# Kernel optimization log

Measured on AMD Instinct MI355X. Metric: run time of the kernel, lower is better.

Reference implementation:

```python
import jax, jax.numpy as jnp
import numpy as np
from jax import lax

NPOINT = 1024
RADIUS = 0.2
NSAMPLE = 32


def fps(xyz, npoint):
    """Furthest point sampling on one cloud. xyz: (N,3) -> (npoint,) int32."""
    n = xyz.shape[0]
    init_d = jnp.full((n,), 1e10, xyz.dtype)

    def body(carry, _):
        dists, last_idx = carry
        last = xyz[last_idx]
        d = jnp.sum((xyz - last) ** 2, axis=-1)
        dists = jnp.minimum(dists, d)
        nxt = jnp.argmax(dists).astype(jnp.int32)
        return (dists, nxt), nxt

    (_, _), idxs = lax.scan(body, (init_d, jnp.int32(0)), None, length=npoint - 1)
    return jnp.concatenate([jnp.zeros((1,), jnp.int32), idxs])


def ball_query(xyz, new_xyz, radius, nsample):
    """First `nsample` points of xyz within `radius` of each center (pad with first hit).
    xyz: (N,3), new_xyz: (S,3) -> (S,nsample) int32."""
    n = xyz.shape[0]
    d2 = jnp.sum((new_xyz[:, None, :] - xyz[None, :, :]) ** 2, axis=-1)  # (S,N)
    cand = jnp.where(d2 < radius * radius, jnp.arange(n, dtype=jnp.int32)[None, :], n)
    idx = jnp.sort(cand, axis=1)[:, :nsample]                            # (S,K)
    first = jnp.where(idx[:, :1] == n, 0, idx[:, :1])
    return jnp.where(idx == n, first, idx)


def setup_inputs() -> dict:
    key = jax.random.key(0)
    ks = jax.random.split(key, 8)
    C_in = 64 + 3  # features + relative xyz
    W1 = jax.random.normal(ks[0], (64, C_in), jnp.float32) * (1.0 / np.sqrt(C_in))
    b1 = jnp.zeros((64,), jnp.float32)
    W2 = jax.random.normal(ks[1], (128, 64), jnp.float32) * (1.0 / np.sqrt(64))
    b2 = jnp.zeros((128,), jnp.float32)
    W3 = jax.random.normal(ks[2], (256, 128), jnp.float32) * (1.0 / np.sqrt(128))
    b3 = jnp.zeros((256,), jnp.float32)
    xyz = jax.random.uniform(ks[3], (8, 4096, 3), jnp.float32)
    features = jax.random.normal(ks[4], (8, 4096, 64), jnp.float32)
    return {"xyz": xyz, "features": features, "W1": W1, "b1": b1,
            "W2": W2, "b2": b2, "W3": W3, "b3": b3}


def reference(xyz, features, W1, b1, W2, b2, W3, b3):
    def per_batch(xyz_b, feat_b):
        fps_idx = fps(xyz_b, NPOINT)                      # (S,)
        new_xyz = xyz_b[fps_idx]                          # (S,3)
        idx = ball_query(xyz_b, new_xyz, RADIUS, NSAMPLE)  # (S,K)
        g_xyz = xyz_b[idx] - new_xyz[:, None, :]          # (S,K,3) relative coords
        g_feat = feat_b[idx]                              # (S,K,C)
        g = jnp.concatenate([g_xyz, g_feat], axis=-1)     # (S,K,3+C)
        x = jnp.transpose(g, (2, 0, 1))                   # (C',S,K)
        for W, b in ((W1, b1), (W2, b2), (W3, b3)):       # 1x1 conv + ReLU stack
            x = jax.nn.relu(jnp.einsum('oc,csk->osk', W, x) + b[:, None, None])
        return new_xyz, jnp.max(x, axis=-1), fps_idx      # max-pool over nsample

    new_xyz, new_features, sample_inds = jax.vmap(per_batch)(xyz, features)
    return new_xyz, new_features, sample_inds
```

## Files before the change

kernel.cpp:

```cpp
#include <hip/hip_runtime.h>
#include <stdint.h>

#define N_PTS 4096
#define S_PTS 1024
#define K_SAMP 32

typedef __attribute__((ext_vector_type(8))) short bf16x8;
typedef __attribute__((ext_vector_type(4))) float f32x4;
typedef __attribute__((ext_vector_type(2))) float f32x2;

#define GT1_S 104
#define GT2_S 72
#define GT3_S 136

__device__ __forceinline__ short f2b(float f){
  unsigned u = __float_as_uint(f);
  u = u + 0x7fffu + ((u >> 16) & 1u);
  return (short)(u >> 16);
}

#define DPP_QUAD_XOR1 0xB1
#define DPP_QUAD_XOR2 0x4E
#define DPP_ROW_HMIRR 0x141
#define DPP_ROW_MIRR  0x140
#define DPP_ROW_BC15  0x142
#define DPP_ROW_BC31  0x143

template<int CTRL>
__device__ __forceinline__ float fstep(float v){
  int o = __builtin_amdgcn_update_dpp(__float_as_int(v), __float_as_int(v),
                                      CTRL, 0xF, 0xF, false);
  return fmaxf(v, __int_as_float(o));
}
template<int CTRL>
__device__ __forceinline__ unsigned ustep(unsigned v){
  unsigned o = (unsigned)__builtin_amdgcn_update_dpp((int)v, (int)v,
                                                     CTRL, 0xF, 0xF, false);
  return o < v ? o : v;
}
__device__ __forceinline__ unsigned long long umax64(unsigned long long a,
                                                     unsigned long long b){
  return a > b ? a : b;
}

__global__ __launch_bounds__(256) void fps_kernel(const float* __restrict__ xyz,
                                                  float* __restrict__ out_newxyz,
                                                  float* __restrict__ out_inds){
#pragma clang fp contract(off)
  __shared__ float4 c4[N_PTS];
  __shared__ float4 logxyz[S_PTS];
  __shared__ __align__(16) unsigned long long slots[2][4];
  const int b = blockIdx.x;
  const int t = threadIdx.x;
  const int lane = t & 63;
  const int w = t >> 6;
  const float* xb = xyz + (size_t)b * N_PTS * 3;

  f32x2 px2[8], py2[8], pz2[8], dist2[8];
#pragma unroll
  for (int j = 0; j < 16; ++j){
    int p = j * 256 + t;
    float x = xb[p*3+0], y = xb[p*3+1], z = xb[p*3+2];
    px2[j>>1][j&1] = x; py2[j>>1][j&1] = y; pz2[j>>1][j&1] = z;
    dist2[j>>1][j&1] = 1e10f;
    c4[p] = make_float4(x, y, z, 0.0f);
  }
  __syncthreads();

  float lx, ly, lz;
  { float4 c0 = c4[0]; lx = c0.x; ly = c0.y; lz = c0.z; }
  if (t == 0) logxyz[0] = make_float4(lx, ly, lz, 0.0f);

  for (int it = 1; it < S_PTS; ++it){
    f32x2 vlx = {lx, lx}, vly = {ly, ly}, vlz = {lz, lz};
    f32x2 bq2[8];
#pragma unroll
    for (int q = 0; q < 8; ++q){
      f32x2 dx = px2[q] - vlx;
      f32x2 dy = py2[q] - vly;
      f32x2 dz = pz2[q] - vlz;
      f32x2 m1 = dx * dx;
      f32x2 m2 = dy * dy;
      f32x2 m3 = dz * dz;
      f32x2 s  = (m1 + m2) + m3;
      f32x2 nd = __builtin_elementwise_min(dist2[q], s);
      dist2[q] = nd;
      bq2[q] = nd;
    }
#pragma unroll
    for (int s = 4; s >= 1; s >>= 1)
#pragma unroll
      for (int q = 0; q < s; ++q)
        bq2[q] = __builtin_elementwise_max(bq2[q], bq2[q+s]);
    float bv = fmaxf(bq2[0][0], bq2[0][1]);

    int idxs[16];
#pragma unroll
    for (int j = 0; j < 16; ++j)
      idxs[j] = (dist2[j>>1][j&1] == bv) ? j : 1024;
#pragma unroll
    for (int s = 8; s >= 1; s >>= 1)
#pragma unroll
      for (int j = 0; j < s; ++j) idxs[j] = min(idxs[j], idxs[j+s]);
    int bi = (idxs[0] << 8) + t;

    float wm = bv;
    wm = fstep<DPP_QUAD_XOR1>(wm);
    wm = fstep<DPP_QUAD_XOR2>(wm);
    wm = fstep<DPP_ROW_HMIRR>(wm);
    wm = fstep<DPP_ROW_MIRR >(wm);
    wm = fstep<DPP_ROW_BC15 >(wm);
    wm = fstep<DPP_ROW_BC31 >(wm);
    float smax = __int_as_float(__builtin_amdgcn_readlane(__float_as_int(wm), 63));

    unsigned long long m = __ballot(bv == smax);
    int wbi;
    if (__popcll(m) == 1){
      wbi = __builtin_amdgcn_readlane(bi, (int)(__ffsll(m) - 1));
    } else {
      unsigned mi = (bv == smax) ? (unsigned)bi : 0xFFFFFFFFu;
      mi = ustep<DPP_QUAD_XOR1>(mi);
      mi = ustep<DPP_QUAD_XOR2>(mi);
      mi = ustep<DPP_ROW_HMIRR>(mi);
      mi = ustep<DPP_ROW_MIRR >(mi);
      mi = ustep<DPP_ROW_BC15 >(mi);
      mi = ustep<DPP_ROW_BC31 >(mi);
      wbi = (int)__builtin_amdgcn_readlane(mi, 63);
    }

    if (lane == 0)
      slots[it & 1][w] = (((unsigned long long)__float_as_uint(smax)) << 32)
                       | (unsigned)(~wbi);
    __syncthreads();

    const unsigned long long* sp = slots[it & 1];
    unsigned long long k0 = sp[0], k1 = sp[1], k2 = sp[2], k3 = sp[3];
    unsigned long long kk = umax64(umax64(k0, k1), umax64(k2, k3));
    int cur = (int)(~(unsigned)kk);

    float4 cc = c4[cur];
    lx = cc.x; ly = cc.y; lz = cc.z;
    if (t == 0) logxyz[it] = make_float4(lx, ly, lz, (float)cur);
  }

  __syncthreads();
#pragma unroll
  for (int k = 0; k < 4; ++k){
    int i = k*256 + t;
    float4 v = logxyz[i];
    out_inds[(size_t)b*S_PTS + i] = v.w;
    out_newxyz[((size_t)b*S_PTS + i)*3 + 0] = v.x;
    out_newxyz[((size_t)b*S_PTS + i)*3 + 1] = v.y;
    out_newxyz[((size_t)b*S_PTS + i)*3 + 2] = v.z;
  }
}

__global__ void wconv_kernel(const float* __restrict__ W1,
                             const float* __restrict__ W2,
                             const float* __restrict__ W3,
                             short* __restrict__ ws_w){
  short* w1 = ws_w;
  short* w2 = ws_w + 64*96;
  short* w3 = ws_w + 64*96 + 128*64;
  int t = blockIdx.x * blockDim.x + threadIdx.x;
  int stride = gridDim.x * blockDim.x;
  for (int i = t; i < 64*96; i += stride){
    int m = i / 96, k = i - m*96;
    float v = 0.0f;
    if (k < 64)      v = W1[m*67 + 3 + k];
    else if (k < 67) v = W1[m*67 + (k - 64)];
    w1[i] = f2b(v);
  }
  for (int i = t; i < 128*64;  i += stride) w2[i] = f2b(W2[i]);
  for (int i = t; i < 256*128; i += stride) w3[i] = f2b(W3[i]);
}

__global__ __launch_bounds__(256) void ballquery_kernel(const float* __restrict__ xyz,
                                                        const float* __restrict__ newxyz,
                                                        int* __restrict__ idx_ws){
  const int lane = threadIdx.x & 63;
  const int c = blockIdx.x * 4 + (threadIdx.x >> 6);
  const int b = c >> 10;
  const float* xb = xyz + (size_t)b * N_PTS * 3;
  const float cx = newxyz[(size_t)c*3+0];
  const float cy = newxyz[(size_t)c*3+1];
  const float cz = newxyz[(size_t)c*3+2];
  const float R2 = 0.2f * 0.2f;
  int* idxp = idx_ws + (size_t)c * K_SAMP;
  int have = 0, first = -1;
  for (int chunk = 0; chunk < 64 && have < K_SAMP; ++chunk){
    int p = chunk * 64 + lane;
    float dx = __fsub_rn(xb[p*3+0], cx);
    float dy = __fsub_rn(xb[p*3+1], cy);
    float dz = __fsub_rn(xb[p*3+2], cz);
    float d2 = __fadd_rn(__fadd_rn(__fmul_rn(dx,dx), __fmul_rn(dy,dy)), __fmul_rn(dz,dz));
    bool hit = d2 < R2;
    unsigned long long mask = __ballot(hit);
    if (mask){
      if (first < 0) first = chunk*64 + (__ffsll(mask) - 1);
      int pre = __popcll(mask & ((1ull << lane) - 1ull));
      if (hit && (have + pre) < K_SAMP) idxp[have + pre] = p;
      have += __popcll(mask);
      if (have > K_SAMP) have = K_SAMP;
    }
  }
  if (first < 0) first = 0;
  if (lane < K_SAMP - have) idxp[have + lane] = first;
}

template<int M, int KC, int KPAD, int GS_IN, int GS_OUT>
__device__ __forceinline__ void layer_mfma(const short* __restrict__ Wl,
                                           const short* gin, short* gout,
                                           const float* __restrict__ sbias_l,
                                           int w, int quad, int col){
  for (int m0 = w*16; m0 < M; m0 += 64){
    f32x4 acc0 = {0,0,0,0}, acc1 = {0,0,0,0};
#pragma unroll
    for (int kc = 0; kc < KC; ++kc){
      bf16x8 a  = *reinterpret_cast<const bf16x8*>(Wl + (size_t)(m0+col)*KPAD + kc*32 + quad*8);
      bf16x8 b0 = *reinterpret_cast<const bf16x8*>(gin + col*GS_IN + kc*32 + quad*8);
      bf16x8 b1 = *reinterpret_cast<const bf16x8*>(gin + (16+col)*GS_IN + kc*32 + quad*8);
      acc0 = __builtin_amdgcn_mfma_f32_16x16x32_bf16(a, b0, acc0, 0, 0, 0);
      acc1 = __builtin_amdgcn_mfma_f32_16x16x32_bf16(a, b1, acc1, 0, 0, 0);
    }
    int rbase = m0 + quad*4;
    unsigned long long P0 = 0ull, P1 = 0ull;
#pragma unroll
    for (int r = 0; r < 4; ++r){
      float bias = sbias_l[rbase + r];
      unsigned long long q0 = (unsigned short)f2b(fmaxf(acc0[r] + bias, 0.0f));
      unsigned long long q1 = (unsigned short)f2b(fmaxf(acc1[r] + bias, 0.0f));
      P0 |= q0 << (16*r);
      P1 |= q1 << (16*r);
    }
    *reinterpret_cast<unsigned long long*>(&gout[col*GS_OUT + rbase])      = P0;
    *reinterpret_cast<unsigned long long*>(&gout[(16+col)*GS_OUT + rbase]) = P1;
  }
}

__global__ __launch_bounds__(256) void mlp_kernel(const float* __restrict__ xyz,
                                                  const float* __restrict__ feat,
                                                  const float* __restrict__ b1,
                                                  const float* __restrict__ b2,
                                                  const float* __restrict__ b3,
                                                  const float* __restrict__ newxyz,
                                                  const int* __restrict__ idx_ws,
                                                  const short* __restrict__ ws_w,
                                                  float* __restrict__ pooled){
  __shared__ __align__(16) short gT1[32*GT1_S];
  __shared__ __align__(16) short gT2[32*GT2_S];
  __shared__ __align__(16) short gT3[32*GT3_S];
  __shared__ int   sidx[32];
  __shared__ float sbias[448];
  const int t = threadIdx.x;
  const int c = blockIdx.x;
  const int b = c >> 10;
  const int lane = t & 63;
  const int w = t >> 6;
  const int quad = lane >> 4;
  const int col = lane & 15;

  const short* w1 = ws_w;
  const short* w2 = ws_w + 64*96;
  const short* w3 = ws_w + 64*96 + 128*64;

  if (t < 32) sidx[t] = idx_ws[(size_t)c*K_SAMP + t];
  for (int i = t; i < 448; i += 256)
    sbias[i] = (i < 64) ? b1[i] : (i < 192) ? b2[i-64] : b3[i-192];
  for (int i = t; i < 32*GT1_S; i += 256) gT1[i] = 0;
  __syncthreads();

  {
    int p = t >> 3, q = t & 7;
    int src = sidx[p];
    const float* fr = feat + ((size_t)b * N_PTS + src) * 64 + q*8;
    unsigned u[4];
#pragma unroll
    for (int jj = 0; jj < 4; ++jj){
      unsigned lo = (unsigned short)f2b(fr[2*jj]);
      unsigned hi = (unsigned short)f2b(fr[2*jj+1]);
      u[jj] = lo | (hi << 16);
    }
    uint4 v; v.x = u[0]; v.y = u[1]; v.z = u[2]; v.w = u[3];
    *reinterpret_cast<uint4*>(&gT1[p*GT1_S + q*8]) = v;
  }
  if (t < 32){
    int src = sidx[t];
    const float* pr = xyz + ((size_t)b * N_PTS + src) * 3;
    float cx = newxyz[(size_t)c*3+0];
    float cy = newxyz[(size_t)c*3+1];
    float cz = newxyz[(size_t)c*3+2];
    gT1[t*GT1_S + 64] = f2b(__fsub_rn(pr[0], cx));
    gT1[t*GT1_S + 65] = f2b(__fsub_rn(pr[1], cy));
    gT1[t*GT1_S + 66] = f2b(__fsub_rn(pr[2], cz));
  }
  __syncthreads();

  layer_mfma<64, 3, 96, GT1_S, GT2_S>(w1, gT1, gT2, sbias, w, quad, col);
  __syncthreads();
  layer_mfma<128, 2, 64, GT2_S, GT3_S>(w2, gT2, gT3, sbias + 64, w, quad, col);
  __syncthreads();

  for (int m0 = w*16; m0 < 256; m0 += 64){
    f32x4 acc0 = {0,0,0,0}, acc1 = {0,0,0,0};
#pragma unroll
    for (int kc = 0; kc < 4; ++kc){
      bf16x8 a  = *reinterpret_cast<const bf16x8*>(w3 + (size_t)(m0+col)*128 + kc*32 + quad*8);
      bf16x8 b0 = *reinterpret_cast<const bf16x8*>(gT3 + col*GT3_S + kc*32 + quad*8);
      bf16x8 b1 = *reinterpret_cast<const bf16x8*>(gT3 + (16+col)*GT3_S + kc*32 + quad*8);
      acc0 = __builtin_amdgcn_mfma_f32_16x16x32_bf16(a, b0, acc0, 0, 0, 0);
      acc1 = __builtin_amdgcn_mfma_f32_16x16x32_bf16(a, b1, acc1, 0, 0, 0);
    }
    float vm[4];
#pragma unroll
    for (int r = 0; r < 4; ++r) vm[r] = fmaxf(acc0[r], acc1[r]);
#pragma unroll
    for (int off = 1; off < 16; off <<= 1){
#pragma unroll
      for (int r = 0; r < 4; ++r) vm[r] = fmaxf(vm[r], __shfl_xor(vm[r], off, 16));
    }
    if (col == 0){
#pragma unroll
      for (int r = 0; r < 4; ++r){
        int ch = m0 + quad*4 + r;
        pooled[(size_t)c*256 + ch] = fmaxf(vm[r] + sbias[192 + ch], 0.0f);
      }
    }
  }
}

__global__ __launch_bounds__(256) void transpose_kernel(const float* __restrict__ pooled,
                                                        float* __restrict__ outf){
  __shared__ float tile[64][65];
  int b  = blockIdx.z;
  int s0 = blockIdx.x * 64;
  int c0 = blockIdx.y * 64;
#pragma unroll
  for (int k = 0; k < 16; ++k){
    int idx = threadIdx.x + k*256;
    int si = idx >> 6, ci = idx & 63;
    tile[si][ci] = pooled[((size_t)b*S_PTS + s0 + si)*256 + c0 + ci];
  }
  __syncthreads();
#pragma unroll
  for (int k = 0; k < 16; ++k){
    int idx = threadIdx.x + k*256;
    int ci = idx >> 6, si = idx & 63;
    outf[((size_t)b*256 + c0 + ci)*S_PTS + s0 + si] = tile[si][ci];
  }
}

extern "C" void kernel_launch(void* const* d_in, const int* in_sizes, int n_in,
                              void* d_out, int out_size, void* d_ws, size_t ws_size,
                              hipStream_t stream){
  const float* xyz  = (const float*)d_in[0];
  const float* feat = (const float*)d_in[1];
  const float* W1   = (const float*)d_in[2];
  const float* b1   = (const float*)d_in[3];
  const float* W2   = (const float*)d_in[4];
  const float* b2   = (const float*)d_in[5];
  const float* W3   = (const float*)d_in[6];
  const float* b3   = (const float*)d_in[7];

  float* out        = (float*)d_out;
  float* out_newxyz = out;
  float* out_feat   = out + 24576;
  float* out_inds   = out + 24576 + 2097152;

  char*  ws     = (char*)d_ws;
  short* ws_w   = (short*)ws;
  int*   idx_ws = (int*)(ws + 94208);
  float* pooled = (float*)(ws + 94208 + 1048576);

  wconv_kernel<<<32, 256, 0, stream>>>(W1, W2, W3, ws_w);
  fps_kernel<<<8, 256, 0, stream>>>(xyz, out_newxyz, out_inds);
  ballquery_kernel<<<2048, 256, 0, stream>>>(xyz, out_newxyz, idx_ws);
  mlp_kernel<<<8192, 256, 0, stream>>>(xyz, feat, b1, b2, b3, out_newxyz,
                                       idx_ws, ws_w, pooled);
  transpose_kernel<<<dim3(16, 4, 8), 256, 0, stream>>>(pooled, out_feat);
}
```

Measured before the change: 820.1 us.

## Replace per-iteration FPS block barrier with tagged LDS slot spin-wait

Each wave in the FPS loop now writes its per-iteration argmax key into a double-buffered LDS slot, tagged with a 10-bit iteration counter and the wave id. The per-iteration __syncthreads is replaced by a spin loop in which each wave polls the four slots until every tag matches the current iteration. The four keys are then reduced with 64-bit DPP quad steps instead of scalar max over LDS reads. The aim is to cut full-block barrier cost on the serial critical path of roughly a thousand iterations. The price is busy-polling on volatile LDS, and correctness depends on the slot contents never accidentally carrying the first iteration's tag.

```diff
diff --git a/kernel.cpp b/kernel.cpp
--- a/kernel.cpp
+++ b/kernel.cpp
@@ -38,9 +38,13 @@
                                                      CTRL, 0xF, 0xF, false);
   return o < v ? o : v;
 }
-__device__ __forceinline__ unsigned long long umax64(unsigned long long a,
-                                                     unsigned long long b){
-  return a > b ? a : b;
+template<int CTRL>
+__device__ __forceinline__ unsigned long long kstep64(unsigned long long k){
+  unsigned lo = (unsigned)k, hi = (unsigned)(k >> 32);
+  unsigned lo2 = (unsigned)__builtin_amdgcn_update_dpp((int)lo, (int)lo, CTRL, 0xF, 0xF, false);
+  unsigned hi2 = (unsigned)__builtin_amdgcn_update_dpp((int)hi, (int)hi, CTRL, 0xF, 0xF, false);
+  unsigned long long ok = ((unsigned long long)hi2 << 32) | lo2;
+  return ok > k ? ok : k;
 }
 
 __global__ __launch_bounds__(256) void fps_kernel(const float* __restrict__ xyz,
@@ -128,15 +132,24 @@
       wbi = (int)__builtin_amdgcn_readlane(mi, 63);
     }
 
-    if (lane == 0)
-      slots[it & 1][w] = (((unsigned long long)__float_as_uint(smax)) << 32)
-                       | (unsigned)(~wbi);
-    __syncthreads();
-
-    const unsigned long long* sp = slots[it & 1];
-    unsigned long long k0 = sp[0], k1 = sp[1], k2 = sp[2], k3 = sp[3];
-    unsigned long long kk = umax64(umax64(k0, k1), umax64(k2, k3));
-    int cur = (int)(~(unsigned)kk);
+    const unsigned tag = (unsigned)(it & 0x3FF);
+    if (lane == 0){
+      unsigned lo = (tag << 15) | ((~(unsigned)wbi & 0xFFFu) << 3) | (unsigned)w;
+      volatile unsigned long long* wp = &slots[it & 1][w];
+      *wp = (((unsigned long long)__float_as_uint(smax)) << 32) | lo;
+    }
+
+    volatile unsigned long long* sp = &slots[it & 1][0];
+    unsigned long long sk;
+    for (;;){
+      sk = sp[lane & 3];
+      unsigned long long rdy = __ballot((((unsigned)sk >> 15) & 0x3FFu) == tag);
+      if (rdy == ~0ull) break;
+    }
+
+    sk = kstep64<DPP_QUAD_XOR1>(sk);
+    sk = kstep64<DPP_QUAD_XOR2>(sk);
+    int cur = (int)((~((unsigned)sk >> 3)) & 0xFFFu);
 
     float4 cc = c4[cur];
     lx = cc.x; ly = cc.y; lz = cc.z;
```

Measured after the change: 868.3 us. 1.06x slower.
